# Performance work log

Measured on AMD Instinct MI355X. Metric: run time of the kernel, lower is better.

Reference implementation:

```python
import jax, jax.numpy as jnp
import numpy as np

BITS = 4        # int4_fullrange
NPACK = 8       # 32-bit container / 4-bit values
BLOCK = 64      # quantization group size (blocksize)
MASK = (1 << BITS) - 1


def _unpack(packed):
    """Unpack int32 words into NPACK 4-bit unsigned values along the last dim.
    packed: (..., P) int32 -> (..., P*NPACK) int32 in [0, 15]."""
    shifts = jnp.arange(NPACK, dtype=jnp.int32) * BITS  # (8,)
    vals = (packed[..., None] >> shifts) & MASK          # (..., P, 8)
    return vals.reshape(*packed.shape[:-1], packed.shape[-1] * NPACK)


def setup_inputs() -> dict:
    key = jax.random.key(0)
    k1, k2, k3, k4, k5 = jax.random.split(key, 5)
    tokens, in_f, out_f = 4096, 4096, 11008
    groups = in_f // BLOCK                      # 64
    x = jax.random.normal(k1, (tokens, in_f), jnp.float32)
    qweight = jax.random.randint(k2, (out_f, in_f // NPACK), 0, 2147483647, jnp.int32)
    qzeros = jax.random.randint(k3, (out_f, groups // NPACK), 0, 2147483647, jnp.int32)
    scales = jax.random.uniform(k4, (out_f, groups), jnp.float32, 0.001, 0.01)
    bias = jax.random.normal(k5, (out_f,), jnp.float32)
    return {"x": x, "qweight": qweight, "qzeros": qzeros, "scales": scales, "bias": bias}


def reference(x, qweight, qzeros, scales, bias):
    # Recover fp32 weight: w[o, g*BLOCK + b] = scales[o, g] * (w_int - zp[o, g])
    out_f, groups = scales.shape
    w_int = _unpack(qweight).astype(jnp.float32)           # (out, in)
    zp = _unpack(qzeros).astype(jnp.float32)               # (out, groups)
    w = (w_int.reshape(out_f, groups, BLOCK) - zp[:, :, None]) * scales[:, :, None]
    w = w.reshape(out_f, groups * BLOCK)                   # (out, in)
    # F.linear(x, w, bias)
    return x @ w.T + bias
```

## Files before the change

kernel.cpp:

```cpp
#include <hip/hip_runtime.h>
#include <stdint.h>

#define M_TOK 4096
#define K_IN  4096
#define N_OUT 11008
#define GROUPS 64
#define WPR 512

#define BM 128
#define BN 128
#define BK 64
#define TILES_M (M_TOK / BM)
#define TILES_N (N_OUT / BN)
#define GN 8

typedef __bf16 bf16x8 __attribute__((ext_vector_type(8)));
typedef float  f32x4  __attribute__((ext_vector_type(4)));

__device__ __forceinline__ uint16_t f2bf(float f) {
  uint32_t u = __float_as_uint(f);
  u += 0x7FFFu + ((u >> 16) & 1u);
  return (uint16_t)(u >> 16);
}

#define XBLK ((M_TOK * K_IN) / (256 * 8))
#define WBLK ((N_OUT * WPR) / 256)

__global__ __launch_bounds__(256) void prep(const float* __restrict__ x,
                                            const uint32_t* __restrict__ qw,
                                            const uint32_t* __restrict__ qz,
                                            const float* __restrict__ sc,
                                            uint16_t* __restrict__ xb,
                                            uint16_t* __restrict__ wb) {
  if (blockIdx.x < XBLK) {
    size_t i = ((size_t)blockIdx.x * 256 + threadIdx.x) * 8;
    const float4* p = (const float4*)(x + i);
    float4 a = p[0];
    float4 b = p[1];
    uint4 v;
    v.x = (uint32_t)f2bf(a.x) | ((uint32_t)f2bf(a.y) << 16);
    v.y = (uint32_t)f2bf(a.z) | ((uint32_t)f2bf(a.w) << 16);
    v.z = (uint32_t)f2bf(b.x) | ((uint32_t)f2bf(b.y) << 16);
    v.w = (uint32_t)f2bf(b.z) | ((uint32_t)f2bf(b.w) << 16);
    *(uint4*)(xb + i) = v;
  } else {
    int idx = (blockIdx.x - XBLK) * 256 + threadIdx.x;
    int o = idx >> 9;
    int p = idx & 511;
    int g = p >> 3;
    uint32_t zw = qz[o * (GROUPS / 8) + (g >> 3)];
    float zp = (float)((zw >> ((g & 7) * 4)) & 15u);
    float s = sc[o * GROUPS + g];
    float c = -s * zp;
    uint32_t w = qw[idx];
    uint4 v;
    uint32_t r[4];
#pragma unroll
    for (int j = 0; j < 4; j++) {
      float f0 = (float)((w >> (8 * j)) & 15u);
      float f1 = (float)((w >> (8 * j + 4)) & 15u);
      r[j] = (uint32_t)f2bf(fmaf(f0, s, c)) | ((uint32_t)f2bf(fmaf(f1, s, c)) << 16);
    }
    v.x = r[0]; v.y = r[1]; v.z = r[2]; v.w = r[3];
    *(uint4*)(wb + (size_t)idx * 8) = v;
  }
}

__global__ __launch_bounds__(256) void gemm_bf16(const uint16_t* __restrict__ A,
                                                 const uint16_t* __restrict__ B,
                                                 const float* __restrict__ bias,
                                                 float* __restrict__ C) {
  __shared__ __align__(16) uint16_t As[BM * BK];
  __shared__ __align__(16) uint16_t Bs[BN * BK];

  int bid = blockIdx.x;
  int nt, mt;
  const int full = (TILES_N / GN) * GN * TILES_M;
  if (bid < full) {
    int group = bid >> 8;
    int rem = bid & 255;
    nt = group * GN + (rem & (GN - 1));
    mt = rem >> 3;
  } else {
    int rem = bid - full;
    nt = (TILES_N / GN) * GN + rem % (TILES_N % GN);
    mt = rem / (TILES_N % GN);
  }
  const int n0 = nt * BN;
  const int m0 = mt * BM;

  const int tid  = threadIdx.x;
  const int wave = tid >> 6;
  const int lane = tid & 63;
  const int wm = wave >> 1;
  const int wn = wave & 1;

  const int lrow = lane >> 3;
  const int lcol = lane & 7;
  const int scol = lcol ^ lrow;

  f32x4 acc[4][4];
#pragma unroll
  for (int i = 0; i < 4; i++)
#pragma unroll
    for (int j = 0; j < 4; j++)
      acc[i][j] = (f32x4){0.f, 0.f, 0.f, 0.f};

  const int col  = lane & 15;
  const int quad = lane >> 4;
  const int cs   = col & 7;

  for (int kt = 0; kt < K_IN / BK; kt++) {
    const int k0 = kt * BK;
#pragma unroll
    for (int c = 0; c < 4; c++) {
      const int br = (c * 4 + wave) * 8;
      const uint16_t* ga = A + (size_t)(m0 + br + lrow) * K_IN + (k0 + scol * 8);
      __builtin_amdgcn_global_load_lds(
          (const __attribute__((address_space(1))) uint32_t*)ga,
          (__attribute__((address_space(3))) uint32_t*)(As + br * BK), 16, 0, 0);
      const uint16_t* gb = B + (size_t)(n0 + br + lrow) * K_IN + (k0 + scol * 8);
      __builtin_amdgcn_global_load_lds(
          (const __attribute__((address_space(1))) uint32_t*)gb,
          (__attribute__((address_space(3))) uint32_t*)(Bs + br * BK), 16, 0, 0);
    }
    __syncthreads();

#pragma unroll
    for (int ki = 0; ki < 2; ki++) {
      bf16x8 af[4], bfr[4];
      const int kc = ki * 4 + quad;
#pragma unroll
      for (int i = 0; i < 4; i++) {
        const int m = wm * 64 + i * 16 + col;
        af[i] = *(const bf16x8*)(As + m * BK + ((kc ^ cs) << 3));
        const int n = wn * 64 + i * 16 + col;
        bfr[i] = *(const bf16x8*)(Bs + n * BK + ((kc ^ cs) << 3));
      }
#pragma unroll
      for (int i = 0; i < 4; i++)
#pragma unroll
        for (int j = 0; j < 4; j++)
          acc[i][j] = __builtin_amdgcn_mfma_f32_16x16x32_bf16(af[i], bfr[j],
                                                              acc[i][j], 0, 0, 0);
    }
    __syncthreads();
  }

#pragma unroll
  for (int i = 0; i < 4; i++) {
#pragma unroll
    for (int j = 0; j < 4; j++) {
      const int n = n0 + wn * 64 + j * 16 + col;
      const int m = m0 + wm * 64 + i * 16 + quad * 4;
      const float bv = bias[n];
      float* out = C + (size_t)m * N_OUT + n;
#pragma unroll
      for (int r = 0; r < 4; r++)
        __builtin_nontemporal_store(acc[i][j][r] + bv, out + (size_t)r * N_OUT);
    }
  }
}

__global__ __launch_bounds__(256) void fallback_fused(const float* __restrict__ x,
                                                      const uint32_t* __restrict__ qw,
                                                      const uint32_t* __restrict__ qz,
                                                      const float* __restrict__ sc,
                                                      const float* __restrict__ bias,
                                                      float* __restrict__ out) {
  __shared__ float xs[K_IN];
  const int t = blockIdx.y;
  const int o = blockIdx.x * 256 + threadIdx.x;
  for (int i = threadIdx.x; i < K_IN; i += 256) xs[i] = x[(size_t)t * K_IN + i];
  __syncthreads();
  float acc = 0.f;
  const uint32_t* qwr = qw + (size_t)o * WPR;
  for (int g = 0; g < GROUPS; g++) {
    uint32_t zw = qz[o * (GROUPS / 8) + (g >> 3)];
    float zp = (float)((zw >> ((g & 7) * 4)) & 15u);
    float s = sc[o * GROUPS + g];
    float gacc = 0.f, gsum = 0.f;
    for (int w = 0; w < 8; w++) {
      uint32_t wv = qwr[g * 8 + w];
#pragma unroll
      for (int j = 0; j < 8; j++) {
        float xv = xs[g * 64 + w * 8 + j];
        gacc = fmaf((float)((wv >> (4 * j)) & 15u), xv, gacc);
        gsum += xv;
      }
    }
    acc += s * (gacc - zp * gsum);
  }
  out[(size_t)t * N_OUT + o] = acc + bias[o];
}

extern "C" void kernel_launch(void* const* d_in, const int* in_sizes, int n_in,
                              void* d_out, int out_size, void* d_ws, size_t ws_size,
                              hipStream_t stream) {
  (void)in_sizes; (void)n_in; (void)out_size;
  const float*    x    = (const float*)d_in[0];
  const uint32_t* qw   = (const uint32_t*)d_in[1];
  const uint32_t* qz   = (const uint32_t*)d_in[2];
  const float*    sc   = (const float*)d_in[3];
  const float*    bias = (const float*)d_in[4];
  float* out = (float*)d_out;

  const size_t xb_bytes = (size_t)M_TOK * K_IN * 2;
  const size_t wb_bytes = (size_t)N_OUT * K_IN * 2;

  if (ws_size >= xb_bytes + wb_bytes) {
    uint16_t* xb = (uint16_t*)d_ws;
    uint16_t* wb = (uint16_t*)((char*)d_ws + xb_bytes);
    prep<<<XBLK + WBLK, 256, 0, stream>>>(x, qw, qz, sc, xb, wb);
    gemm_bf16<<<TILES_N * TILES_M, 256, 0, stream>>>(xb, wb, bias, out);
  } else {
    fallback_fused<<<dim3(N_OUT / 256, M_TOK), 256, 0, stream>>>(x, qw, qz, sc, bias, out);
  }
}
```

Baseline: 700.6 us.

## Rewrite bf16 GEMM as 256x256 tile, 8-wave double-buffered ping-pong pipeline

Replaces the 128x128 single-buffered GEMM with a 256x256 tile computed by 512 threads (8 waves). It uses double-buffered LDS and splits each K-tile into quarter stages that interleave async global-to-LDS loads with MFMA work, using explicit barriers, waitcnts, sched_barriers and setprio. Tile ordering is also changed to an 8-way interleaved mapping. The aim is to hide global load latency and raise arithmetic intensity per LDS byte, at the cost of 128KB of LDS per block (one block per CU) and a fragile hand-written synchronization schedule.

```diff
diff --git a/kernel.cpp b/kernel.cpp
--- a/kernel.cpp
+++ b/kernel.cpp
@@ -7,12 +7,13 @@
 #define GROUPS 64
 #define WPR 512
 
-#define BM 128
-#define BN 128
+#define BM 256
+#define BN 256
 #define BK 64
-#define TILES_M (M_TOK / BM)
-#define TILES_N (N_OUT / BN)
-#define GN 8
+#define TM (M_TOK / BM)
+#define TN (N_OUT / BN)
+#define NWG (TM * TN)
+#define KTILES (K_IN / BK)
 
 typedef __bf16 bf16x8 __attribute__((ext_vector_type(8)));
 typedef float  f32x4  __attribute__((ext_vector_type(4)));
@@ -66,95 +67,194 @@
   }
 }
 
-__global__ __launch_bounds__(256) void gemm_bf16(const uint16_t* __restrict__ A,
-                                                 const uint16_t* __restrict__ B,
-                                                 const float* __restrict__ bias,
-                                                 float* __restrict__ C) {
-  __shared__ __align__(16) uint16_t As[BM * BK];
-  __shared__ __align__(16) uint16_t Bs[BN * BK];
-
-  int bid = blockIdx.x;
-  int nt, mt;
-  const int full = (TILES_N / GN) * GN * TILES_M;
-  if (bid < full) {
-    int group = bid >> 8;
-    int rem = bid & 255;
-    nt = group * GN + (rem & (GN - 1));
-    mt = rem >> 3;
-  } else {
-    int rem = bid - full;
-    nt = (TILES_N / GN) * GN + rem % (TILES_N % GN);
-    mt = rem / (TILES_N % GN);
-  }
-  const int n0 = nt * BN;
-  const int m0 = mt * BM;
+#define SBAR()   __builtin_amdgcn_s_barrier()
+#define SCHED0() __builtin_amdgcn_sched_barrier(0)
+#define WAITV(n) asm volatile("s_waitcnt vmcnt(" #n ")" ::: "memory")
+#define WAITL0() asm volatile("s_waitcnt lgkmcnt(0)" ::: "memory")
+
+#define STAGE_A(buf, half, kt) do {                                            \
+  _Pragma("unroll")                                                            \
+  for (int c_ = 0; c_ < 2; c_++) {                                             \
+    const int r_ = (half) * 128 + c_ * 64 + wave * 8;                          \
+    __builtin_amdgcn_global_load_lds(                                          \
+        (const __attribute__((address_space(1))) uint32_t*)(                   \
+            gA + (size_t)r_ * K_IN + (size_t)(kt) * BK),                       \
+        (__attribute__((address_space(3))) uint32_t*)(&As[(buf)][r_][0]),      \
+        16, 0, 0);                                                             \
+  } } while (0)
+
+#define STAGE_B(buf, half, kt) do {                                            \
+  _Pragma("unroll")                                                            \
+  for (int c_ = 0; c_ < 2; c_++) {                                             \
+    const int r_ = (half) * 128 + c_ * 64 + wave * 8;                          \
+    __builtin_amdgcn_global_load_lds(                                          \
+        (const __attribute__((address_space(1))) uint32_t*)(                   \
+            gB + (size_t)r_ * K_IN + (size_t)(kt) * BK),                       \
+        (__attribute__((address_space(3))) uint32_t*)(&Bs[(buf)][r_][0]),      \
+        16, 0, 0);                                                             \
+  } } while (0)
+
+#define LOAD_A(buf, mh) do {                                                   \
+  _Pragma("unroll")                                                            \
+  for (int i2_ = 0; i2_ < 4; i2_++) {                                          \
+    const int row_ = (mh) * 128 + wm * 64 + i2_ * 16 + col;                    \
+    af[i2_][0] = *(const bf16x8*)&As[(buf)][row_][(quad ^ cs) << 3];           \
+    af[i2_][1] = *(const bf16x8*)&As[(buf)][row_][((4 + quad) ^ cs) << 3];     \
+  } } while (0)
+
+#define LOAD_B(buf, nh) do {                                                   \
+  _Pragma("unroll")                                                            \
+  for (int j2_ = 0; j2_ < 2; j2_++) {                                          \
+    const int row_ = (nh) * 128 + wn * 32 + j2_ * 16 + col;                    \
+    bfr[j2_][0] = *(const bf16x8*)&Bs[(buf)][row_][(quad ^ cs) << 3];          \
+    bfr[j2_][1] = *(const bf16x8*)&Bs[(buf)][row_][((4 + quad) ^ cs) << 3];    \
+  } } while (0)
+
+#define MMA(mh, nh) do {                                                       \
+  __builtin_amdgcn_s_setprio(1);                                               \
+  _Pragma("unroll")                                                            \
+  for (int i2_ = 0; i2_ < 4; i2_++)                                            \
+    _Pragma("unroll")                                                          \
+    for (int j2_ = 0; j2_ < 2; j2_++) {                                        \
+      acc[(mh)*4 + i2_][(nh)*2 + j2_] = __builtin_amdgcn_mfma_f32_16x16x32_bf16( \
+          af[i2_][0], bfr[j2_][0], acc[(mh)*4 + i2_][(nh)*2 + j2_], 0, 0, 0);  \
+      acc[(mh)*4 + i2_][(nh)*2 + j2_] = __builtin_amdgcn_mfma_f32_16x16x32_bf16( \
+          af[i2_][1], bfr[j2_][1], acc[(mh)*4 + i2_][(nh)*2 + j2_], 0, 0, 0);  \
+    }                                                                          \
+  __builtin_amdgcn_s_setprio(0); } while (0)
+
+__global__ __launch_bounds__(512, 2) void gemm_bf16(const uint16_t* __restrict__ A,
+                                                    const uint16_t* __restrict__ B,
+                                                    const float* __restrict__ bias,
+                                                    float* __restrict__ C) {
+  __shared__ __align__(16) uint16_t As[2][BM][BK];
+  __shared__ __align__(16) uint16_t Bs[2][BN][BK];
+
+  const int bid = blockIdx.x;
+  const int wg  = (bid & 7) * (NWG / 8) + (bid >> 3);
+  const int mt  = wg / TN;
+  const int nt  = wg % TN;
+  const size_t m0 = (size_t)mt * BM;
+  const size_t n0 = (size_t)nt * BN;
 
   const int tid  = threadIdx.x;
   const int wave = tid >> 6;
   const int lane = tid & 63;
-  const int wm = wave >> 1;
-  const int wn = wave & 1;
-
+  const int wm   = wave >> 2;
+  const int wn   = wave & 3;
   const int lrow = lane >> 3;
   const int lcol = lane & 7;
-  const int scol = lcol ^ lrow;
-
-  f32x4 acc[4][4];
-#pragma unroll
-  for (int i = 0; i < 4; i++)
-#pragma unroll
-    for (int j = 0; j < 4; j++)
-      acc[i][j] = (f32x4){0.f, 0.f, 0.f, 0.f};
-
   const int col  = lane & 15;
   const int quad = lane >> 4;
   const int cs   = col & 7;
 
-  for (int kt = 0; kt < K_IN / BK; kt++) {
-    const int k0 = kt * BK;
-#pragma unroll
-    for (int c = 0; c < 4; c++) {
-      const int br = (c * 4 + wave) * 8;
-      const uint16_t* ga = A + (size_t)(m0 + br + lrow) * K_IN + (k0 + scol * 8);
-      __builtin_amdgcn_global_load_lds(
-          (const __attribute__((address_space(1))) uint32_t*)ga,
-          (__attribute__((address_space(3))) uint32_t*)(As + br * BK), 16, 0, 0);
-      const uint16_t* gb = B + (size_t)(n0 + br + lrow) * K_IN + (k0 + scol * 8);
-      __builtin_amdgcn_global_load_lds(
-          (const __attribute__((address_space(1))) uint32_t*)gb,
-          (__attribute__((address_space(3))) uint32_t*)(Bs + br * BK), 16, 0, 0);
-    }
-    __syncthreads();
-
-#pragma unroll
-    for (int ki = 0; ki < 2; ki++) {
-      bf16x8 af[4], bfr[4];
-      const int kc = ki * 4 + quad;
-#pragma unroll
-      for (int i = 0; i < 4; i++) {
-        const int m = wm * 64 + i * 16 + col;
-        af[i] = *(const bf16x8*)(As + m * BK + ((kc ^ cs) << 3));
-        const int n = wn * 64 + i * 16 + col;
-        bfr[i] = *(const bf16x8*)(Bs + n * BK + ((kc ^ cs) << 3));
-      }
-#pragma unroll
-      for (int i = 0; i < 4; i++)
-#pragma unroll
-        for (int j = 0; j < 4; j++)
-          acc[i][j] = __builtin_amdgcn_mfma_f32_16x16x32_bf16(af[i], bfr[j],
-                                                              acc[i][j], 0, 0, 0);
-    }
-    __syncthreads();
-  }
-
-#pragma unroll
-  for (int i = 0; i < 4; i++) {
+  const uint16_t* gA = A + (m0 + lrow) * K_IN + (size_t)((lcol ^ lrow) << 3);
+  const uint16_t* gB = B + (n0 + lrow) * K_IN + (size_t)((lcol ^ lrow) << 3);
+
+  f32x4 acc[8][4];
+#pragma unroll
+  for (int i = 0; i < 8; i++)
+#pragma unroll
+    for (int j = 0; j < 4; j++)
+      acc[i][j] = (f32x4){0.f, 0.f, 0.f, 0.f};
+
+  bf16x8 af[4][2];
+  bf16x8 bfr[2][2];
+
+  STAGE_A(0, 0, 0); STAGE_B(0, 1, 0); STAGE_A(0, 1, 0); STAGE_B(0, 0, 0);
+  STAGE_A(1, 0, 1); STAGE_B(1, 1, 1);
+  WAITV(4);
+  SBAR(); SCHED0();
+
+  for (int it = 0; it < KTILES / 2 - 1; ++it) {
+    const int kt = 2 * it;
+    LOAD_A(0, 0); LOAD_B(0, 0);
+    STAGE_A(1, 1, kt + 1);
+    SBAR(); WAITL0(); SCHED0();
+    MMA(0, 0);
+    SBAR(); SCHED0();
+    LOAD_B(0, 1);
+    STAGE_B(1, 0, kt + 1);
+    SBAR(); WAITL0(); SCHED0();
+    MMA(0, 1);
+    SBAR(); SCHED0();
+    LOAD_A(0, 1);
+    STAGE_A(0, 0, kt + 2);
+    SBAR(); WAITL0(); SCHED0();
+    MMA(1, 1);
+    SBAR(); SCHED0();
+    LOAD_B(0, 0);
+    STAGE_B(0, 1, kt + 2);
+    SBAR(); WAITL0(); SCHED0();
+    MMA(1, 0);
+    WAITV(4);
+    SBAR(); SCHED0();
+    LOAD_A(1, 0); LOAD_B(1, 0);
+    STAGE_A(0, 1, kt + 2);
+    SBAR(); WAITL0(); SCHED0();
+    MMA(0, 0);
+    SBAR(); SCHED0();
+    LOAD_B(1, 1);
+    STAGE_B(0, 0, kt + 2);
+    SBAR(); WAITL0(); SCHED0();
+    MMA(0, 1);
+    SBAR(); SCHED0();
+    LOAD_A(1, 1);
+    STAGE_A(1, 0, kt + 3);
+    SBAR(); WAITL0(); SCHED0();
+    MMA(1, 1);
+    SBAR(); SCHED0();
+    LOAD_B(1, 0);
+    STAGE_B(1, 1, kt + 3);
+    SBAR(); WAITL0(); SCHED0();
+    MMA(1, 0);
+    WAITV(4);
+    SBAR(); SCHED0();
+  }
+
+  LOAD_A(0, 0); LOAD_B(0, 0);
+  STAGE_A(1, 1, KTILES - 1);
+  SBAR(); WAITL0(); SCHED0();
+  MMA(0, 0);
+  SBAR(); SCHED0();
+  LOAD_B(0, 1);
+  STAGE_B(1, 0, KTILES - 1);
+  SBAR(); WAITL0(); SCHED0();
+  MMA(0, 1);
+  SBAR(); SCHED0();
+  LOAD_A(0, 1);
+  SBAR(); WAITL0(); SCHED0();
+  MMA(1, 1);
+  SBAR(); SCHED0();
+  LOAD_B(0, 0);
+  SBAR(); WAITL0(); SCHED0();
+  MMA(1, 0);
+  WAITV(0);
+  SBAR(); SCHED0();
+  LOAD_A(1, 0); LOAD_B(1, 0);
+  SBAR(); WAITL0(); SCHED0();
+  MMA(0, 0);
+  SBAR(); SCHED0();
+  LOAD_B(1, 1);
+  SBAR(); WAITL0(); SCHED0();
+  MMA(0, 1);
+  SBAR(); SCHED0();
+  LOAD_A(1, 1);
+  SBAR(); WAITL0(); SCHED0();
+  MMA(1, 1);
+  SBAR(); SCHED0();
+  LOAD_B(1, 0);
+  SBAR(); WAITL0(); SCHED0();
+  MMA(1, 0);
+
+#pragma unroll
+  for (int i = 0; i < 8; i++) {
+    const int mrow = (int)m0 + (i >> 2) * 128 + wm * 64 + (i & 3) * 16 + quad * 4;
 #pragma unroll
     for (int j = 0; j < 4; j++) {
-      const int n = n0 + wn * 64 + j * 16 + col;
-      const int m = m0 + wm * 64 + i * 16 + quad * 4;
-      const float bv = bias[n];
-      float* out = C + (size_t)m * N_OUT + n;
+      const int ncol = (int)n0 + (j >> 1) * 128 + wn * 32 + (j & 1) * 16 + col;
+      const float bv = bias[ncol];
+      float* out = C + (size_t)mrow * N_OUT + ncol;
 #pragma unroll
       for (int r = 0; r < 4; r++)
         __builtin_nontemporal_store(acc[i][j][r] + bv, out + (size_t)r * N_OUT);
@@ -212,7 +312,7 @@
     uint16_t* xb = (uint16_t*)d_ws;
     uint16_t* wb = (uint16_t*)((char*)d_ws + xb_bytes);
     prep<<<XBLK + WBLK, 256, 0, stream>>>(x, qw, qz, sc, xb, wb);
-    gemm_bf16<<<TILES_N * TILES_M, 256, 0, stream>>>(xb, wb, bias, out);
+    gemm_bf16<<<NWG, 512, 0, stream>>>(xb, wb, bias, out);
   } else {
     fallback_fused<<<dim3(N_OUT / 256, M_TOK), 256, 0, stream>>>(x, qw, qz, sc, bias, out);
   }
```

New measurement: 633.7 us. 1.11x faster.
